# Kernel tuning notes

Measured on AMD Instinct MI355X. Metric: run time of the kernel, lower is better.

## Reference

```python
import jax, jax.numpy as jnp
import numpy as np

D_MODEL = 512
D_PROJ = 32
N_CENT = 6
CORR_HIDDEN = max(D_MODEL // 16, 32)  # 32
LN_EPS = 1e-5
ALPHA_DIR = 5.0


def _layernorm(x, g, b):
    mu = x.mean(axis=-1, keepdims=True)
    var = jnp.mean((x - mu) ** 2, axis=-1, keepdims=True)
    return (x - mu) * jax.lax.rsqrt(var + LN_EPS) * g + b


def _l2norm(x, eps=1e-12):
    n = jnp.sqrt(jnp.sum(x * x, axis=-1, keepdims=True))
    return x / jnp.maximum(n, eps)


def setup_inputs() -> dict:
    key = jax.random.key(0)
    ks = jax.random.split(key, 8)
    B, N = 64, 1024
    x = jax.random.normal(ks[0], (B, N, D_MODEL), dtype=jnp.float32)
    s_in = 1.0 / np.sqrt(D_MODEL)
    proj_w = jax.random.uniform(ks[1], (D_PROJ, D_MODEL), jnp.float32, -s_in, s_in)
    proj_b = jax.random.uniform(ks[2], (D_PROJ,), jnp.float32, -s_in, s_in)
    ln_g = jnp.ones((D_PROJ,), jnp.float32)
    ln_b = jnp.zeros((D_PROJ,), jnp.float32)
    centroids = jax.random.uniform(ks[3], (N_CENT, D_PROJ), jnp.float32, -3.0, 3.0)
    s_c = 1.0 / np.sqrt(D_MODEL + D_PROJ)
    corr_in_w = jax.random.uniform(ks[4], (CORR_HIDDEN, D_MODEL + D_PROJ), jnp.float32, -s_c, s_c)
    corr_in_b = jax.random.uniform(ks[5], (CORR_HIDDEN,), jnp.float32, -s_c, s_c)
    # correction_out is zero-init in the module; use small random values so the
    # correction path is numerically exercised by the baseline.
    corr_out_w = jax.random.normal(ks[6], (D_MODEL, CORR_HIDDEN), jnp.float32) * 0.02
    corr_out_b = jax.random.normal(ks[7], (D_MODEL,), jnp.float32) * 0.02
    return {
        "x": x, "proj_w": proj_w, "proj_b": proj_b, "ln_g": ln_g, "ln_b": ln_b,
        "centroids": centroids,
        "corr_in_w": corr_in_w, "corr_in_b": corr_in_b,
        "corr_out_w": corr_out_w, "corr_out_b": corr_out_b,
        "gate_alpha": jnp.float32(0.0),
        "routing_log_temp": jnp.float32(1.6),
        "scale_evidence": jnp.float32(5.0),
    }


def reference(x, proj_w, proj_b, ln_g, ln_b, centroids, corr_in_w, corr_in_b,
              corr_out_w, corr_out_b, gate_alpha, routing_log_temp, scale_evidence):
    B, N, D = x.shape
    # per-variate RevIN-style normalization over the variate axis (dim=1), unbiased std
    rev_mean = x.mean(axis=1, keepdims=True)
    rev_var = jnp.sum((x - rev_mean) ** 2, axis=1, keepdims=True) / (N - 1)
    rev_std = jnp.sqrt(rev_var) + 1e-5
    x_norm = (x - rev_mean) / rev_std
    # geometric routing: proj -> LN -> cosine sim against centroids
    Q = _layernorm(jnp.einsum("bnd,pd->bnp", x_norm, proj_w) + proj_b, ln_g, ln_b)
    Q_n = _l2norm(Q)                      # [B,N,P]
    K_n = _l2norm(centroids)              # [K,P]
    sim_cos = jnp.einsum("bnp,kp->bnk", Q_n, K_n)
    soft_assign = jax.nn.softmax(sim_cos * jnp.exp(routing_log_temp), axis=-1)
    centroid_ctx = jnp.einsum("bnk,kp->bnp", soft_assign, centroids)
    # centroid-conditioned correction MLP (dropout is identity in eval)
    corr_input = jnp.concatenate([x_norm, centroid_ctx], axis=-1)  # [B,N,D+P]
    h = jax.nn.gelu(jnp.einsum("bnc,hc->bnh", corr_input, corr_in_w) + corr_in_b, approximate=False)
    correction = (jnp.einsum("bnh,dh->bnd", h, corr_out_w) + corr_out_b) * rev_std
    gate = jax.nn.sigmoid(gate_alpha)
    out = x + gate * correction
    # DST uncertainty (no-grad diagnostic)
    sim_ctrl = jax.lax.stop_gradient(sim_cos)
    dir_gate = jax.nn.softplus((sim_ctrl - sim_ctrl.mean(axis=-1, keepdims=True)) * ALPHA_DIR)
    s_ev = jax.nn.softplus(jax.lax.stop_gradient(scale_evidence))
    S_train = jnp.sum(dir_gate * s_ev + 1.0, axis=-1, keepdims=True)
    u_std = N_CENT / S_train
    # losses
    gram = K_n @ K_n.T
    ortho_loss = jnp.mean((gram - jnp.eye(N_CENT, dtype=x.dtype)) ** 2)
    avg_routing = soft_assign.mean(axis=(0, 1))
    latent_loss = jnp.mean((avg_routing - 1.0 / N_CENT) ** 2)
    return out, u_std, ortho_loss, latent_loss
```

## Files before the change

kernel.cpp:

```cpp
#include <hip/hip_runtime.h>
#include <cstdint>
#include <cstddef>

#define N_DIM 1024
#define D_DIM 512
#define M_DIM 65536
#define NC 6

typedef float f32x4 __attribute__((ext_vector_type(4)));
typedef __bf16 bf16x8 __attribute__((ext_vector_type(8)));

__device__ __forceinline__ float sp_f(float z) {
    return z > 20.f ? z : log1pf(expf(z));
}

__global__ void k_pack(const float* __restrict__ pw, const float* __restrict__ ciw,
                       const float* __restrict__ cow, const float* __restrict__ cent,
                       const float* __restrict__ ga, const float* __restrict__ rlt,
                       const float* __restrict__ sev,
                       __bf16* __restrict__ bpa, __bf16* __restrict__ bpl,
                       __bf16* __restrict__ w3p,
                       float* __restrict__ kn, float* __restrict__ cw,
                       float* __restrict__ scal, float* __restrict__ out_ortho) {
    __shared__ float skn[NC * 32];
    __shared__ float ssq[36];
    int bid = blockIdx.x, tid = threadIdx.x;
    if (bid < 128) {
        int i = bid * 256 + tid;
        int c = i >> 9, k = i & 511;
        float w = (c < 32) ? pw[c * 512 + k] : ciw[(c - 32) * 544 + k];
        __bf16 hi = (__bf16)w;
        bpa[i] = hi;
        if (c < 32) bpl[i] = (__bf16)(w - (float)hi);
    } else if (bid < 192) {
        int j = (bid - 128) * 256 + tid;
        w3p[j] = (__bf16)cow[j];
    } else if (bid == 192) {
        if (tid < 192) {
            int k = tid >> 5, h = tid & 31;
            float s = 0.f;
            for (int p = 0; p < 32; ++p) s += cent[k * 32 + p] * ciw[h * 544 + 512 + p];
            cw[k * 32 + h] = s;
        } else if (tid < 192 + NC) {
            int k = tid - 192;
            float s = 0.f;
            for (int p = 0; p < 32; ++p) { float v = cent[k * 32 + p]; s += v * v; }
            float inv = 1.f / fmaxf(sqrtf(s), 1e-12f);
            for (int p = 0; p < 32; ++p) kn[k * 32 + p] = cent[k * 32 + p] * inv;
        } else if (tid == 198) {
            scal[0] = expf(rlt[0]);
            scal[1] = sp_f(sev[0]);
            scal[2] = 1.f / (1.f + expf(-ga[0]));
        }
    } else {
        if (tid < NC) {
            float s = 0.f;
            for (int p = 0; p < 32; ++p) { float v = cent[tid * 32 + p]; s += v * v; }
            float inv = 1.f / fmaxf(sqrtf(s), 1e-12f);
            for (int p = 0; p < 32; ++p) skn[tid * 32 + p] = cent[tid * 32 + p] * inv;
        }
        __syncthreads();
        if (tid < 36) {
            int i = tid / 6, j = tid % 6;
            float g = 0.f;
            for (int p = 0; p < 32; ++p) g += skn[i * 32 + p] * skn[j * 32 + p];
            float d = g - (i == j ? 1.f : 0.f);
            ssq[tid] = d * d;
        }
        __syncthreads();
        if (tid == 0) {
            float s = 0.f;
            for (int i = 0; i < 36; ++i) s += ssq[i];
            *out_ortho = s / 36.f;
        }
    }
}

__global__ void k_stat1(const float* __restrict__ x, float* __restrict__ part) {
    int bid = blockIdx.x;
    int b = bid >> 5, sub = bid & 31;
    int d4 = threadIdx.x * 4;
    const float* px = x + ((size_t)(b * 1024 + sub * 32)) * 512 + d4;
    f32x4 s = {0.f, 0.f, 0.f, 0.f}, q = s;
    #pragma unroll 8
    for (int i = 0; i < 32; ++i) {
        float4 v = *(const float4*)(px + (size_t)i * 512);
        s.x += v.x; s.y += v.y; s.z += v.z; s.w += v.w;
        q.x += v.x * v.x; q.y += v.y * v.y; q.z += v.z * v.z; q.w += v.w * v.w;
    }
    *(f32x4*)(part + (size_t)bid * 512 + d4) = s;
    *(f32x4*)(part + (size_t)(2048 + bid) * 512 + d4) = q;
}

__global__ void k_stat2(const float* __restrict__ part, float* __restrict__ mean,
                        float* __restrict__ istd, float* __restrict__ stdv) {
    int b = blockIdx.x, d = threadIdx.x;
    float s = 0.f, q = 0.f;
    for (int c = 0; c < 32; ++c) {
        s += part[(size_t)(b * 32 + c) * 512 + d];
        q += part[(size_t)(2048 + b * 32 + c) * 512 + d];
    }
    float mu = s * (1.f / (float)N_DIM);
    float var = fmaxf((q - s * mu) * (1.f / (float)(N_DIM - 1)), 0.f);
    float sd = sqrtf(var) + 1e-5f;
    mean[b * D_DIM + d] = mu;
    istd[b * D_DIM + d] = 1.f / sd;
    stdv[b * D_DIM + d] = sd;
}

__launch_bounds__(256)
__global__ void mega(const float* __restrict__ x,
                     const float* __restrict__ proj_b, const float* __restrict__ ln_g,
                     const float* __restrict__ ln_b, const float* __restrict__ cib,
                     const float* __restrict__ cob,
                     const float* __restrict__ mean, const float* __restrict__ istd,
                     const float* __restrict__ stdv,
                     const float* __restrict__ kn, const float* __restrict__ cw,
                     const float* __restrict__ scal,
                     const __bf16* __restrict__ bpa, const __bf16* __restrict__ bpl,
                     const __bf16* __restrict__ w3p,
                     float* __restrict__ out, float* __restrict__ ustd_out,
                     float* __restrict__ rout_part) {
    __shared__ float s_mean[512];
    __shared__ float s_is[512];
    __shared__ float s_sd[512];
    __shared__ float s_cob[512];
    __shared__ __align__(16) float s_tile[2][16][68];
    __shared__ __align__(16) __bf16 s_h[2][16][40];

    int tid = threadIdx.x;
    int wv = tid >> 6, ln = tid & 63;
    int l15 = ln & 15, lg = ln >> 4;
    int pair = wv >> 1, h = wv & 1;

    int b = blockIdx.x >> 5;
    int wrow = blockIdx.x * 32 + pair * 16;

    if (tid < 128) {
        *(float4*)&s_mean[tid * 4] = *(const float4*)(mean + b * 512 + tid * 4);
        *(float4*)&s_sd[tid * 4]   = *(const float4*)(stdv + b * 512 + tid * 4);
    } else {
        int t = tid - 128;
        *(float4*)&s_is[t * 4]  = *(const float4*)(istd + b * 512 + t * 4);
        *(float4*)&s_cob[t * 4] = *(const float4*)(cob + t * 4);
    }
    __syncthreads();

    int kbase = h * 256;
    const float* xr = x + (size_t)(wrow + l15) * 512 + kbase;
    const __bf16* w0  = bpa + (size_t)l15 * 512 + kbase;
    const __bf16* w1  = bpa + (size_t)(16 + l15) * 512 + kbase;
    const __bf16* w2  = bpa + (size_t)(32 + l15) * 512 + kbase;
    const __bf16* w3  = bpa + (size_t)(48 + l15) * 512 + kbase;
    const __bf16* wl0 = bpl + (size_t)l15 * 512 + kbase;
    const __bf16* wl1 = bpl + (size_t)(16 + l15) * 512 + kbase;

    f32x4 a0 = {0.f, 0.f, 0.f, 0.f}, a1 = a0, a2 = a0, a3 = a0;
    #pragma unroll
    for (int ks = 0; ks < 8; ++ks) {
        int k0 = ks * 32 + lg * 8;
        int kk = kbase + k0;
        float4 xa = *(const float4*)(xr + k0);
        float4 xb = *(const float4*)(xr + k0 + 4);
        float4 ma = *(const float4*)&s_mean[kk];
        float4 m2 = *(const float4*)&s_mean[kk + 4];
        float4 ia = *(const float4*)&s_is[kk];
        float4 i2 = *(const float4*)&s_is[kk + 4];
        float xnf[8];
        xnf[0] = (xa.x - ma.x) * ia.x; xnf[1] = (xa.y - ma.y) * ia.y;
        xnf[2] = (xa.z - ma.z) * ia.z; xnf[3] = (xa.w - ma.w) * ia.w;
        xnf[4] = (xb.x - m2.x) * i2.x; xnf[5] = (xb.y - m2.y) * i2.y;
        xnf[6] = (xb.z - m2.z) * i2.z; xnf[7] = (xb.w - m2.w) * i2.w;
        bf16x8 ah, al;
        #pragma unroll
        for (int j = 0; j < 8; ++j) {
            __bf16 hh = (__bf16)xnf[j];
            ah[j] = hh;
            al[j] = (__bf16)(xnf[j] - (float)hh);
        }
        bf16x8 wh0 = *(const bf16x8*)(w0 + k0);
        bf16x8 wh1 = *(const bf16x8*)(w1 + k0);
        a0 = __builtin_amdgcn_mfma_f32_16x16x32_bf16(ah, wh0, a0, 0, 0, 0);
        a0 = __builtin_amdgcn_mfma_f32_16x16x32_bf16(ah, *(const bf16x8*)(wl0 + k0), a0, 0, 0, 0);
        a0 = __builtin_amdgcn_mfma_f32_16x16x32_bf16(al, wh0, a0, 0, 0, 0);
        a1 = __builtin_amdgcn_mfma_f32_16x16x32_bf16(ah, wh1, a1, 0, 0, 0);
        a1 = __builtin_amdgcn_mfma_f32_16x16x32_bf16(ah, *(const bf16x8*)(wl1 + k0), a1, 0, 0, 0);
        a1 = __builtin_amdgcn_mfma_f32_16x16x32_bf16(al, wh1, a1, 0, 0, 0);
        a2 = __builtin_amdgcn_mfma_f32_16x16x32_bf16(ah, *(const bf16x8*)(w2 + k0), a2, 0, 0, 0);
        a3 = __builtin_amdgcn_mfma_f32_16x16x32_bf16(ah, *(const bf16x8*)(w3 + k0), a3, 0, 0, 0);
    }

    if (h == 1) {
        #pragma unroll
        for (int rg = 0; rg < 4; ++rg) {
            int row = lg * 4 + rg;
            s_tile[pair][row][l15]      = a0[rg];
            s_tile[pair][row][16 + l15] = a1[rg];
            s_tile[pair][row][32 + l15] = a2[rg];
            s_tile[pair][row][48 + l15] = a3[rg];
        }
    }
    __syncthreads();

    if (h == 0) {
        #pragma unroll
        for (int rg = 0; rg < 4; ++rg) {
            int row = lg * 4 + rg;
            s_tile[pair][row][l15]      += a0[rg];
            s_tile[pair][row][16 + l15] += a1[rg];
            s_tile[pair][row][32 + l15] += a2[rg];
            s_tile[pair][row][48 + l15] += a3[rg];
        }

        int r = ln >> 2, sub = ln & 3;
        const float* tr = &s_tile[pair][r][0];
        float4 t0 = *(const float4*)(tr + sub * 8);
        float4 t1 = *(const float4*)(tr + sub * 8 + 4);
        float4 pb0 = *(const float4*)(proj_b + sub * 8);
        float4 pb1 = *(const float4*)(proj_b + sub * 8 + 4);
        float P[8];
        P[0] = t0.x + pb0.x; P[1] = t0.y + pb0.y; P[2] = t0.z + pb0.z; P[3] = t0.w + pb0.w;
        P[4] = t1.x + pb1.x; P[5] = t1.y + pb1.y; P[6] = t1.z + pb1.z; P[7] = t1.w + pb1.w;
        float m = 0.f;
        #pragma unroll
        for (int j = 0; j < 8; ++j) m += P[j];
        m += __shfl_xor(m, 1); m += __shfl_xor(m, 2);
        float mu = m * (1.f / 32.f);
        float v = 0.f;
        #pragma unroll
        for (int j = 0; j < 8; ++j) { float d = P[j] - mu; v += d * d; }
        v += __shfl_xor(v, 1); v += __shfl_xor(v, 2);
        float rs = rsqrtf(v * (1.f / 32.f) + 1e-5f);
        float4 g0 = *(const float4*)(ln_g + sub * 8);
        float4 g1 = *(const float4*)(ln_g + sub * 8 + 4);
        float4 bl0 = *(const float4*)(ln_b + sub * 8);
        float4 bl1 = *(const float4*)(ln_b + sub * 8 + 4);
        float gg[8] = {g0.x, g0.y, g0.z, g0.w, g1.x, g1.y, g1.z, g1.w};
        float bb[8] = {bl0.x, bl0.y, bl0.z, bl0.w, bl1.x, bl1.y, bl1.z, bl1.w};
        float q[8]; float n2 = 0.f;
        #pragma unroll
        for (int j = 0; j < 8; ++j) {
            q[j] = (P[j] - mu) * rs * gg[j] + bb[j];
            n2 += q[j] * q[j];
        }
        n2 += __shfl_xor(n2, 1); n2 += __shfl_xor(n2, 2);
        float inv = 1.f / fmaxf(sqrtf(n2), 1e-12f);
        float sim[6];
        #pragma unroll
        for (int k = 0; k < 6; ++k) {
            const float* kr = kn + k * 32 + sub * 8;
            float4 ka = *(const float4*)(kr);
            float4 kb = *(const float4*)(kr + 4);
            float s = q[0] * ka.x + q[1] * ka.y + q[2] * ka.z + q[3] * ka.w
                    + q[4] * kb.x + q[5] * kb.y + q[6] * kb.z + q[7] * kb.w;
            s += __shfl_xor(s, 1); s += __shfl_xor(s, 2);
            sim[k] = s * inv;
        }
        float T = scal[0], sevv = scal[1];
        float mx = sim[0];
        #pragma unroll
        for (int k = 1; k < 6; ++k) mx = fmaxf(mx, sim[k]);
        float e[6], es = 0.f;
        #pragma unroll
        for (int k = 0; k < 6; ++k) { e[k] = expf((sim[k] - mx) * T); es += e[k]; }
        float einv = 1.f / es;
        float a[6];
        #pragma unroll
        for (int k = 0; k < 6; ++k) a[k] = e[k] * einv;
        float msim = 0.f;
        #pragma unroll
        for (int k = 0; k < 6; ++k) msim += sim[k];
        msim *= (1.f / 6.f);
        float S = 6.f;
        #pragma unroll
        for (int k = 0; k < 6; ++k) S += sevv * sp_f((sim[k] - msim) * 5.f);
        if (sub == 0) ustd_out[wrow + r] = 6.f / S;
        float4 h0 = *(const float4*)(tr + 32 + sub * 8);
        float4 h1 = *(const float4*)(tr + 32 + sub * 8 + 4);
        float4 c0 = *(const float4*)(cib + sub * 8);
        float4 c1 = *(const float4*)(cib + sub * 8 + 4);
        float vh[8] = {h0.x + c0.x, h0.y + c0.y, h0.z + c0.z, h0.w + c0.w,
                       h1.x + c1.x, h1.y + c1.y, h1.z + c1.z, h1.w + c1.w};
        #pragma unroll
        for (int k = 0; k < 6; ++k) {
            const float* cr = cw + k * 32 + sub * 8;
            float4 ca = *(const float4*)(cr);
            float4 cb = *(const float4*)(cr + 4);
            vh[0] += a[k] * ca.x; vh[1] += a[k] * ca.y; vh[2] += a[k] * ca.z; vh[3] += a[k] * ca.w;
            vh[4] += a[k] * cb.x; vh[5] += a[k] * cb.y; vh[6] += a[k] * cb.z; vh[7] += a[k] * cb.w;
        }
        bf16x8 hv;
        #pragma unroll
        for (int j = 0; j < 8; ++j) {
            float gv = 0.5f * vh[j] * (1.f + erff(vh[j] * 0.70710678118654752f));
            hv[j] = (__bf16)gv;
        }
        *(bf16x8*)(&s_h[pair][r][sub * 8]) = hv;
        #pragma unroll
        for (int k = 0; k < 6; ++k) {
            float rv = (sub == 0) ? a[k] : 0.f;
            rv += __shfl_xor(rv, 4); rv += __shfl_xor(rv, 8);
            rv += __shfl_xor(rv, 16); rv += __shfl_xor(rv, 32);
            if (ln == 0) atomicAdd(rout_part + (blockIdx.x & 63) * 6 + k, rv);
        }
    }
    __syncthreads();

    bf16x8 ha = *(const bf16x8*)(&s_h[pair][l15][lg * 8]);
    float gate = scal[2];
    int nf0 = h * 16;
    int row = wrow + l15;
    for (int nf = nf0; nf < nf0 + 16; ++nf) {
        int col = nf * 16 + l15;
        bf16x8 wb = *(const bf16x8*)(w3p + col * 32 + lg * 8);
        f32x4 z = {0.f, 0.f, 0.f, 0.f};
        f32x4 d = __builtin_amdgcn_mfma_f32_16x16x32_bf16(wb, ha, z, 0, 0, 0);
        int colb = nf * 16 + lg * 4;
        float4 xv = *(const float4*)(x + (size_t)row * 512 + colb);
        float4 bi = *(const float4*)&s_cob[colb];
        float4 sd = *(const float4*)&s_sd[colb];
        float4 o;
        o.x = xv.x + gate * ((d[0] + bi.x) * sd.x);
        o.y = xv.y + gate * ((d[1] + bi.y) * sd.y);
        o.z = xv.z + gate * ((d[2] + bi.z) * sd.z);
        o.w = xv.w + gate * ((d[3] + bi.w) * sd.w);
        *(float4*)(out + (size_t)row * 512 + colb) = o;
    }
}

__global__ void k5(const float* __restrict__ rp, float* __restrict__ out_latent) {
    __shared__ float sv[6];
    int t = threadIdx.x;
    if (t < 6) {
        float s = 0.f;
        for (int i = 0; i < 64; ++i) s += rp[i * 6 + t];
        sv[t] = s;
    }
    __syncthreads();
    if (t == 0) {
        float s = 0.f;
        for (int k = 0; k < 6; ++k) {
            float av = sv[k] * (1.f / (float)M_DIM) - (1.f / 6.f);
            s += av * av;
        }
        *out_latent = s / 6.f;
    }
}

extern "C" void kernel_launch(void* const* d_in, const int* in_sizes, int n_in,
                              void* d_out, int out_size, void* d_ws, size_t ws_size,
                              hipStream_t stream) {
    const float* x      = (const float*)d_in[0];
    const float* proj_w = (const float*)d_in[1];
    const float* proj_b = (const float*)d_in[2];
    const float* ln_g   = (const float*)d_in[3];
    const float* ln_b   = (const float*)d_in[4];
    const float* cent   = (const float*)d_in[5];
    const float* ciw    = (const float*)d_in[6];
    const float* cib    = (const float*)d_in[7];
    const float* cow    = (const float*)d_in[8];
    const float* cob    = (const float*)d_in[9];
    const float* ga     = (const float*)d_in[10];
    const float* rlt    = (const float*)d_in[11];
    const float* sev    = (const float*)d_in[12];

    char* ws = (char*)d_ws;
    float*  rout = (float*)(ws + 0);
    float*  kn   = (float*)(ws + 2048);
    float*  cwv  = (float*)(ws + 4096);
    float*  scal = (float*)(ws + 6144);
    __bf16* bpa  = (__bf16*)(ws + 8192);
    __bf16* bpl  = (__bf16*)(ws + 73728);
    __bf16* w3p  = (__bf16*)(ws + 106496);
    float*  mean = (float*)(ws + 139264);
    float*  istd = (float*)(ws + 270336);
    float*  stdv = (float*)(ws + 401408);

    float* outp   = (float*)d_out;
    float* ustd   = outp + (size_t)M_DIM * D_DIM;
    float* ortho  = ustd + M_DIM;
    float* latent = ortho + 1;

    float* part = (float*)d_out;

    hipMemsetAsync(rout, 0, 64 * 6 * sizeof(float), stream);
    k_pack<<<194, 256, 0, stream>>>(proj_w, ciw, cow, cent, ga, rlt, sev,
                                    bpa, bpl, w3p, kn, cwv, scal, ortho);
    k_stat1<<<2048, 128, 0, stream>>>(x, part);
    k_stat2<<<64, 512, 0, stream>>>(part, mean, istd, stdv);
    mega<<<2048, 256, 0, stream>>>(x, proj_b, ln_g, ln_b, cib, cob,
                                   mean, istd, stdv, kn, cwv, scal,
                                   bpa, bpl, w3p, outp, ustd, rout);
    k5<<<1, 64, 0, stream>>>(rout, latent);
}
```

Baseline: 140.3 us.

## Split K across four waves per 16-row tile and double grid size

Each block now handles 16 rows rather than 32. All four waves split the 512-wide K dimension of the projection GEMM, 128 columns each, and the partial results are reduced in shared memory by wave 0. The output stage spreads the 32 column fragments across the four waves and fully unrolls the loop. The grid doubles to 4096 blocks to raise parallelism and shorten per-wave serial work, at the cost of more per-block overhead: staging the per-batch stats again, extra syncs, and wave 0 doing the LayerNorm/routing tail alone while the other waves idle.

```diff
diff --git a/kernel.cpp b/kernel.cpp
--- a/kernel.cpp
+++ b/kernel.cpp
@@ -125,16 +125,15 @@
     __shared__ float s_is[512];
     __shared__ float s_sd[512];
     __shared__ float s_cob[512];
-    __shared__ __align__(16) float s_tile[2][16][68];
-    __shared__ __align__(16) __bf16 s_h[2][16][40];
+    __shared__ __align__(16) float s_t[3][16][68];
+    __shared__ __align__(16) __bf16 s_h[16][40];
 
     int tid = threadIdx.x;
     int wv = tid >> 6, ln = tid & 63;
     int l15 = ln & 15, lg = ln >> 4;
-    int pair = wv >> 1, h = wv & 1;
-
-    int b = blockIdx.x >> 5;
-    int wrow = blockIdx.x * 32 + pair * 16;
+
+    int b = blockIdx.x >> 6;
+    int wrow = blockIdx.x * 16;
 
     if (tid < 128) {
         *(float4*)&s_mean[tid * 4] = *(const float4*)(mean + b * 512 + tid * 4);
@@ -146,7 +145,7 @@
     }
     __syncthreads();
 
-    int kbase = h * 256;
+    int kbase = wv * 128;
     const float* xr = x + (size_t)(wrow + l15) * 512 + kbase;
     const __bf16* w0  = bpa + (size_t)l15 * 512 + kbase;
     const __bf16* w1  = bpa + (size_t)(16 + l15) * 512 + kbase;
@@ -157,7 +156,7 @@
 
     f32x4 a0 = {0.f, 0.f, 0.f, 0.f}, a1 = a0, a2 = a0, a3 = a0;
     #pragma unroll
-    for (int ks = 0; ks < 8; ++ks) {
+    for (int ks = 0; ks < 4; ++ks) {
         int k0 = ks * 32 + lg * 8;
         int kk = kbase + k0;
         float4 xa = *(const float4*)(xr + k0);
@@ -190,30 +189,35 @@
         a3 = __builtin_amdgcn_mfma_f32_16x16x32_bf16(ah, *(const bf16x8*)(w3 + k0), a3, 0, 0, 0);
     }
 
-    if (h == 1) {
+    if (wv != 0) {
+        int j = wv - 1;
         #pragma unroll
         for (int rg = 0; rg < 4; ++rg) {
             int row = lg * 4 + rg;
-            s_tile[pair][row][l15]      = a0[rg];
-            s_tile[pair][row][16 + l15] = a1[rg];
-            s_tile[pair][row][32 + l15] = a2[rg];
-            s_tile[pair][row][48 + l15] = a3[rg];
+            s_t[j][row][l15]      = a0[rg];
+            s_t[j][row][16 + l15] = a1[rg];
+            s_t[j][row][32 + l15] = a2[rg];
+            s_t[j][row][48 + l15] = a3[rg];
         }
     }
     __syncthreads();
 
-    if (h == 0) {
+    if (wv == 0) {
         #pragma unroll
         for (int rg = 0; rg < 4; ++rg) {
             int row = lg * 4 + rg;
-            s_tile[pair][row][l15]      += a0[rg];
-            s_tile[pair][row][16 + l15] += a1[rg];
-            s_tile[pair][row][32 + l15] += a2[rg];
-            s_tile[pair][row][48 + l15] += a3[rg];
+            a0[rg] += s_t[0][row][l15]      + s_t[1][row][l15]      + s_t[2][row][l15];
+            a1[rg] += s_t[0][row][16 + l15] + s_t[1][row][16 + l15] + s_t[2][row][16 + l15];
+            a2[rg] += s_t[0][row][32 + l15] + s_t[1][row][32 + l15] + s_t[2][row][32 + l15];
+            a3[rg] += s_t[0][row][48 + l15] + s_t[1][row][48 + l15] + s_t[2][row][48 + l15];
+            s_t[0][row][l15]      = a0[rg];
+            s_t[0][row][16 + l15] = a1[rg];
+            s_t[0][row][32 + l15] = a2[rg];
+            s_t[0][row][48 + l15] = a3[rg];
         }
 
         int r = ln >> 2, sub = ln & 3;
-        const float* tr = &s_tile[pair][r][0];
+        const float* tr = &s_t[0][r][0];
         float4 t0 = *(const float4*)(tr + sub * 8);
         float4 t1 = *(const float4*)(tr + sub * 8 + 4);
         float4 pb0 = *(const float4*)(proj_b + sub * 8);
@@ -295,7 +299,7 @@
             float gv = 0.5f * vh[j] * (1.f + erff(vh[j] * 0.70710678118654752f));
             hv[j] = (__bf16)gv;
         }
-        *(bf16x8*)(&s_h[pair][r][sub * 8]) = hv;
+        *(bf16x8*)(&s_h[r][sub * 8]) = hv;
         #pragma unroll
         for (int k = 0; k < 6; ++k) {
             float rv = (sub == 0) ? a[k] : 0.f;
@@ -306,25 +310,28 @@
     }
     __syncthreads();
 
-    bf16x8 ha = *(const bf16x8*)(&s_h[pair][l15][lg * 8]);
+    bf16x8 ha = *(const bf16x8*)(&s_h[l15][lg * 8]);
     float gate = scal[2];
-    int nf0 = h * 16;
     int row = wrow + l15;
-    for (int nf = nf0; nf < nf0 + 16; ++nf) {
+    const float* xrow = x + (size_t)row * 512;
+    float* orow = out + (size_t)row * 512;
+    #pragma unroll
+    for (int i = 0; i < 8; ++i) {
+        int nf = wv * 8 + i;
         int col = nf * 16 + l15;
         bf16x8 wb = *(const bf16x8*)(w3p + col * 32 + lg * 8);
         f32x4 z = {0.f, 0.f, 0.f, 0.f};
         f32x4 d = __builtin_amdgcn_mfma_f32_16x16x32_bf16(wb, ha, z, 0, 0, 0);
         int colb = nf * 16 + lg * 4;
-        float4 xv = *(const float4*)(x + (size_t)row * 512 + colb);
+        float4 xv = *(const float4*)(xrow + colb);
         float4 bi = *(const float4*)&s_cob[colb];
         float4 sd = *(const float4*)&s_sd[colb];
-        float4 o;
-        o.x = xv.x + gate * ((d[0] + bi.x) * sd.x);
-        o.y = xv.y + gate * ((d[1] + bi.y) * sd.y);
-        o.z = xv.z + gate * ((d[2] + bi.z) * sd.z);
-        o.w = xv.w + gate * ((d[3] + bi.w) * sd.w);
-        *(float4*)(out + (size_t)row * 512 + colb) = o;
+        f32x4 o;
+        o[0] = xv.x + gate * ((d[0] + bi.x) * sd.x);
+        o[1] = xv.y + gate * ((d[1] + bi.y) * sd.y);
+        o[2] = xv.z + gate * ((d[2] + bi.z) * sd.z);
+        o[3] = xv.w + gate * ((d[3] + bi.w) * sd.w);
+        *(f32x4*)(orow + colb) = o;
     }
 }
 
@@ -388,7 +395,7 @@
                                     bpa, bpl, w3p, kn, cwv, scal, ortho);
     k_stat1<<<2048, 128, 0, stream>>>(x, part);
     k_stat2<<<64, 512, 0, stream>>>(part, mean, istd, stdv);
-    mega<<<2048, 256, 0, stream>>>(x, proj_b, ln_g, ln_b, cib, cob,
+    mega<<<4096, 256, 0, stream>>>(x, proj_b, ln_g, ln_b, cib, cob,
                                    mean, istd, stdv, kn, cwv, scal,
                                    bpa, bpl, w3p, outp, ustd, rout);
     k5<<<1, 64, 0, stream>>>(rout, latent);
```

After: 146.4 us. +4.4%, slower.

## Fold RevIN normalization into per-batch weights and bias, precompute gated epilogue scales

Applied to the files above, without the earlier changes.

Adds a k_pack2 kernel that scales the projection and correction-input weights by each batch's inverse std and folds the mean term into per-batch bias vectors. The mega kernel can then feed raw x into the MFMAs without the per-element subtract and multiply, and its epilogue uses precomputed sd*gate and cob*sd*gate. Small constants (kn, cw, ln params, scalars) are staged in shared memory. The cost is an extra launch and a per-batch copy of the weights (about 4 MB of bf16) that mega must read, which means fewer cache hits across batches, plus a change in rounding because x is split into hi/lo before normalization.

```diff
diff --git a/kernel.cpp b/kernel.cpp
--- a/kernel.cpp
+++ b/kernel.cpp
@@ -18,24 +18,16 @@
                        const float* __restrict__ cow, const float* __restrict__ cent,
                        const float* __restrict__ ga, const float* __restrict__ rlt,
                        const float* __restrict__ sev,
-                       __bf16* __restrict__ bpa, __bf16* __restrict__ bpl,
-                       __bf16* __restrict__ w3p,
-                       float* __restrict__ kn, float* __restrict__ cw,
-                       float* __restrict__ scal, float* __restrict__ out_ortho) {
+                       __bf16* __restrict__ w3p, float* __restrict__ kn,
+                       float* __restrict__ cw, float* __restrict__ scal,
+                       float* __restrict__ out_ortho) {
     __shared__ float skn[NC * 32];
     __shared__ float ssq[36];
     int bid = blockIdx.x, tid = threadIdx.x;
-    if (bid < 128) {
-        int i = bid * 256 + tid;
-        int c = i >> 9, k = i & 511;
-        float w = (c < 32) ? pw[c * 512 + k] : ciw[(c - 32) * 544 + k];
-        __bf16 hi = (__bf16)w;
-        bpa[i] = hi;
-        if (c < 32) bpl[i] = (__bf16)(w - (float)hi);
-    } else if (bid < 192) {
-        int j = (bid - 128) * 256 + tid;
+    if (bid < 64) {
+        int j = bid * 256 + tid;
         w3p[j] = (__bf16)cow[j];
-    } else if (bid == 192) {
+    } else if (bid == 64) {
         if (tid < 192) {
             int k = tid >> 5, h = tid & 31;
             float s = 0.f;
@@ -108,23 +100,73 @@
     stdv[b * D_DIM + d] = sd;
 }
 
+__global__ void k_pack2(const float* __restrict__ pw, const float* __restrict__ ciw,
+                        const float* __restrict__ proj_b, const float* __restrict__ cib,
+                        const float* __restrict__ cob,
+                        const float* __restrict__ mean, const float* __restrict__ istd,
+                        const float* __restrict__ stdv, const float* __restrict__ scal,
+                        __bf16* __restrict__ bpa2, __bf16* __restrict__ bpl2,
+                        float* __restrict__ c2g, float* __restrict__ sdg,
+                        float* __restrict__ bsg) {
+    __shared__ float s_mi[512];
+    __shared__ float s_part[4][64];
+    int bid = blockIdx.x, tid = threadIdx.x;
+    int b = bid / 7, part = bid % 7;
+    if (part < 6) {
+        #pragma unroll
+        for (int r = 0; r < 16; ++r) {
+            int cc = part * 16 + r;
+            for (int k = tid; k < 512; k += 256) {
+                float is = istd[b * 512 + k];
+                if (cc < 64) {
+                    float w = (cc < 32) ? pw[cc * 512 + k] : ciw[(cc - 32) * 544 + k];
+                    bpa2[((size_t)b * 64 + cc) * 512 + k] = (__bf16)(w * is);
+                } else {
+                    int c0 = cc - 64;
+                    float v = pw[c0 * 512 + k] * is;
+                    __bf16 hi = (__bf16)v;
+                    bpl2[((size_t)b * 32 + c0) * 512 + k] = (__bf16)(v - (float)hi);
+                }
+            }
+        }
+    } else {
+        float g = scal[2];
+        for (int k = tid; k < 512; k += 256) {
+            s_mi[k] = mean[b * 512 + k] * istd[b * 512 + k];
+            float sd = stdv[b * 512 + k];
+            sdg[b * 512 + k] = sd * g;
+            bsg[b * 512 + k] = cob[k] * sd * g;
+        }
+        __syncthreads();
+        int col = tid & 63, seg = tid >> 6;
+        float s = 0.f;
+        for (int k = seg * 128; k < seg * 128 + 128; ++k) {
+            float w = (col < 32) ? pw[col * 512 + k] : ciw[(col - 32) * 544 + k];
+            s += s_mi[k] * w;
+        }
+        s_part[seg][col] = s;
+        __syncthreads();
+        if (tid < 64) {
+            float bias = (tid < 32) ? proj_b[tid] : cib[tid - 32];
+            c2g[b * 64 + tid] = bias - (s_part[0][tid] + s_part[1][tid] +
+                                        s_part[2][tid] + s_part[3][tid]);
+        }
+    }
+}
+
 __launch_bounds__(256)
 __global__ void mega(const float* __restrict__ x,
-                     const float* __restrict__ proj_b, const float* __restrict__ ln_g,
-                     const float* __restrict__ ln_b, const float* __restrict__ cib,
-                     const float* __restrict__ cob,
-                     const float* __restrict__ mean, const float* __restrict__ istd,
-                     const float* __restrict__ stdv,
+                     const float* __restrict__ ln_g, const float* __restrict__ ln_b,
                      const float* __restrict__ kn, const float* __restrict__ cw,
-                     const float* __restrict__ scal,
-                     const __bf16* __restrict__ bpa, const __bf16* __restrict__ bpl,
+                     const float* __restrict__ scal, const float* __restrict__ c2g,
+                     const float* __restrict__ sdg, const float* __restrict__ bsg,
+                     const __bf16* __restrict__ bpa2, const __bf16* __restrict__ bpl2,
                      const __bf16* __restrict__ w3p,
                      float* __restrict__ out, float* __restrict__ ustd_out,
                      float* __restrict__ rout_part) {
-    __shared__ float s_mean[512];
-    __shared__ float s_is[512];
-    __shared__ float s_sd[512];
-    __shared__ float s_cob[512];
+    __shared__ float s_sdg[512];
+    __shared__ float s_bsg[512];
+    __shared__ float s_kn[192], s_cw[192], s_c2[64], s_g[32], s_bl[32], s_scal[3];
     __shared__ __align__(16) float s_tile[2][16][68];
     __shared__ __align__(16) __bf16 s_h[2][16][40];
 
@@ -137,46 +179,42 @@
     int wrow = blockIdx.x * 32 + pair * 16;
 
     if (tid < 128) {
-        *(float4*)&s_mean[tid * 4] = *(const float4*)(mean + b * 512 + tid * 4);
-        *(float4*)&s_sd[tid * 4]   = *(const float4*)(stdv + b * 512 + tid * 4);
+        *(float4*)&s_sdg[tid * 4] = *(const float4*)(sdg + b * 512 + tid * 4);
+        if (tid < 48)       *(float4*)&s_kn[tid * 4] = *(const float4*)(kn + tid * 4);
+        else if (tid < 96)  *(float4*)&s_cw[(tid - 48) * 4] = *(const float4*)(cw + (tid - 48) * 4);
+        else if (tid < 112) *(float4*)&s_c2[(tid - 96) * 4] = *(const float4*)(c2g + b * 64 + (tid - 96) * 4);
+        else if (tid < 120) *(float4*)&s_g[(tid - 112) * 4] = *(const float4*)(ln_g + (tid - 112) * 4);
+        else                *(float4*)&s_bl[(tid - 120) * 4] = *(const float4*)(ln_b + (tid - 120) * 4);
     } else {
-        int t = tid - 128;
-        *(float4*)&s_is[t * 4]  = *(const float4*)(istd + b * 512 + t * 4);
-        *(float4*)&s_cob[t * 4] = *(const float4*)(cob + t * 4);
+        *(float4*)&s_bsg[(tid - 128) * 4] = *(const float4*)(bsg + b * 512 + (tid - 128) * 4);
+        if (tid == 128) { s_scal[0] = scal[0]; s_scal[1] = scal[1]; s_scal[2] = scal[2]; }
     }
     __syncthreads();
 
     int kbase = h * 256;
     const float* xr = x + (size_t)(wrow + l15) * 512 + kbase;
-    const __bf16* w0  = bpa + (size_t)l15 * 512 + kbase;
-    const __bf16* w1  = bpa + (size_t)(16 + l15) * 512 + kbase;
-    const __bf16* w2  = bpa + (size_t)(32 + l15) * 512 + kbase;
-    const __bf16* w3  = bpa + (size_t)(48 + l15) * 512 + kbase;
-    const __bf16* wl0 = bpl + (size_t)l15 * 512 + kbase;
-    const __bf16* wl1 = bpl + (size_t)(16 + l15) * 512 + kbase;
+    const __bf16* wbase = bpa2 + ((size_t)b * 64) * 512 + kbase;
+    const __bf16* w0 = wbase + (size_t)l15 * 512;
+    const __bf16* w1 = wbase + (size_t)(16 + l15) * 512;
+    const __bf16* w2 = wbase + (size_t)(32 + l15) * 512;
+    const __bf16* w3 = wbase + (size_t)(48 + l15) * 512;
+    const __bf16* lbase = bpl2 + ((size_t)b * 32) * 512 + kbase;
+    const __bf16* wl0 = lbase + (size_t)l15 * 512;
+    const __bf16* wl1 = lbase + (size_t)(16 + l15) * 512;
 
     f32x4 a0 = {0.f, 0.f, 0.f, 0.f}, a1 = a0, a2 = a0, a3 = a0;
     #pragma unroll
     for (int ks = 0; ks < 8; ++ks) {
         int k0 = ks * 32 + lg * 8;
-        int kk = kbase + k0;
         float4 xa = *(const float4*)(xr + k0);
         float4 xb = *(const float4*)(xr + k0 + 4);
-        float4 ma = *(const float4*)&s_mean[kk];
-        float4 m2 = *(const float4*)&s_mean[kk + 4];
-        float4 ia = *(const float4*)&s_is[kk];
-        float4 i2 = *(const float4*)&s_is[kk + 4];
-        float xnf[8];
-        xnf[0] = (xa.x - ma.x) * ia.x; xnf[1] = (xa.y - ma.y) * ia.y;
-        xnf[2] = (xa.z - ma.z) * ia.z; xnf[3] = (xa.w - ma.w) * ia.w;
-        xnf[4] = (xb.x - m2.x) * i2.x; xnf[5] = (xb.y - m2.y) * i2.y;
-        xnf[6] = (xb.z - m2.z) * i2.z; xnf[7] = (xb.w - m2.w) * i2.w;
+        float xf[8] = {xa.x, xa.y, xa.z, xa.w, xb.x, xb.y, xb.z, xb.w};
         bf16x8 ah, al;
         #pragma unroll
         for (int j = 0; j < 8; ++j) {
-            __bf16 hh = (__bf16)xnf[j];
+            __bf16 hh = (__bf16)xf[j];
             ah[j] = hh;
-            al[j] = (__bf16)(xnf[j] - (float)hh);
+            al[j] = (__bf16)(xf[j] - (float)hh);
         }
         bf16x8 wh0 = *(const bf16x8*)(w0 + k0);
         bf16x8 wh1 = *(const bf16x8*)(w1 + k0);
@@ -216,11 +254,11 @@
         const float* tr = &s_tile[pair][r][0];
         float4 t0 = *(const float4*)(tr + sub * 8);
         float4 t1 = *(const float4*)(tr + sub * 8 + 4);
-        float4 pb0 = *(const float4*)(proj_b + sub * 8);
-        float4 pb1 = *(const float4*)(proj_b + sub * 8 + 4);
+        float4 c2a = *(const float4*)&s_c2[sub * 8];
+        float4 c2b = *(const float4*)&s_c2[sub * 8 + 4];
         float P[8];
-        P[0] = t0.x + pb0.x; P[1] = t0.y + pb0.y; P[2] = t0.z + pb0.z; P[3] = t0.w + pb0.w;
-        P[4] = t1.x + pb1.x; P[5] = t1.y + pb1.y; P[6] = t1.z + pb1.z; P[7] = t1.w + pb1.w;
+        P[0] = t0.x + c2a.x; P[1] = t0.y + c2a.y; P[2] = t0.z + c2a.z; P[3] = t0.w + c2a.w;
+        P[4] = t1.x + c2b.x; P[5] = t1.y + c2b.y; P[6] = t1.z + c2b.z; P[7] = t1.w + c2b.w;
         float m = 0.f;
         #pragma unroll
         for (int j = 0; j < 8; ++j) m += P[j];
@@ -231,10 +269,10 @@
         for (int j = 0; j < 8; ++j) { float d = P[j] - mu; v += d * d; }
         v += __shfl_xor(v, 1); v += __shfl_xor(v, 2);
         float rs = rsqrtf(v * (1.f / 32.f) + 1e-5f);
-        float4 g0 = *(const float4*)(ln_g + sub * 8);
-        float4 g1 = *(const float4*)(ln_g + sub * 8 + 4);
-        float4 bl0 = *(const float4*)(ln_b + sub * 8);
-        float4 bl1 = *(const float4*)(ln_b + sub * 8 + 4);
+        float4 g0 = *(const float4*)&s_g[sub * 8];
+        float4 g1 = *(const float4*)&s_g[sub * 8 + 4];
+        float4 bl0 = *(const float4*)&s_bl[sub * 8];
+        float4 bl1 = *(const float4*)&s_bl[sub * 8 + 4];
         float gg[8] = {g0.x, g0.y, g0.z, g0.w, g1.x, g1.y, g1.z, g1.w};
         float bb[8] = {bl0.x, bl0.y, bl0.z, bl0.w, bl1.x, bl1.y, bl1.z, bl1.w};
         float q[8]; float n2 = 0.f;
@@ -248,7 +286,7 @@
         float sim[6];
         #pragma unroll
         for (int k = 0; k < 6; ++k) {
-            const float* kr = kn + k * 32 + sub * 8;
+            const float* kr = &s_kn[k * 32 + sub * 8];
             float4 ka = *(const float4*)(kr);
             float4 kb = *(const float4*)(kr + 4);
             float s = q[0] * ka.x + q[1] * ka.y + q[2] * ka.z + q[3] * ka.w
@@ -256,7 +294,7 @@
             s += __shfl_xor(s, 1); s += __shfl_xor(s, 2);
             sim[k] = s * inv;
         }
-        float T = scal[0], sevv = scal[1];
+        float T = s_scal[0], sevv = s_scal[1];
         float mx = sim[0];
         #pragma unroll
         for (int k = 1; k < 6; ++k) mx = fmaxf(mx, sim[k]);
@@ -277,13 +315,13 @@
         if (sub == 0) ustd_out[wrow + r] = 6.f / S;
         float4 h0 = *(const float4*)(tr + 32 + sub * 8);
         float4 h1 = *(const float4*)(tr + 32 + sub * 8 + 4);
-        float4 c0 = *(const float4*)(cib + sub * 8);
-        float4 c1 = *(const float4*)(cib + sub * 8 + 4);
+        float4 c0 = *(const float4*)&s_c2[32 + sub * 8];
+        float4 c1 = *(const float4*)&s_c2[32 + sub * 8 + 4];
         float vh[8] = {h0.x + c0.x, h0.y + c0.y, h0.z + c0.z, h0.w + c0.w,
                        h1.x + c1.x, h1.y + c1.y, h1.z + c1.z, h1.w + c1.w};
         #pragma unroll
         for (int k = 0; k < 6; ++k) {
-            const float* cr = cw + k * 32 + sub * 8;
+            const float* cr = &s_cw[k * 32 + sub * 8];
             float4 ca = *(const float4*)(cr);
             float4 cb = *(const float4*)(cr + 4);
             vh[0] += a[k] * ca.x; vh[1] += a[k] * ca.y; vh[2] += a[k] * ca.z; vh[3] += a[k] * ca.w;
@@ -307,7 +345,6 @@
     __syncthreads();
 
     bf16x8 ha = *(const bf16x8*)(&s_h[pair][l15][lg * 8]);
-    float gate = scal[2];
     int nf0 = h * 16;
     int row = wrow + l15;
     for (int nf = nf0; nf < nf0 + 16; ++nf) {
@@ -317,14 +354,14 @@
         f32x4 d = __builtin_amdgcn_mfma_f32_16x16x32_bf16(wb, ha, z, 0, 0, 0);
         int colb = nf * 16 + lg * 4;
         float4 xv = *(const float4*)(x + (size_t)row * 512 + colb);
-        float4 bi = *(const float4*)&s_cob[colb];
-        float4 sd = *(const float4*)&s_sd[colb];
-        float4 o;
-        o.x = xv.x + gate * ((d[0] + bi.x) * sd.x);
-        o.y = xv.y + gate * ((d[1] + bi.y) * sd.y);
-        o.z = xv.z + gate * ((d[2] + bi.z) * sd.z);
-        o.w = xv.w + gate * ((d[3] + bi.w) * sd.w);
-        *(float4*)(out + (size_t)row * 512 + colb) = o;
+        float4 sg = *(const float4*)&s_sdg[colb];
+        float4 bg = *(const float4*)&s_bsg[colb];
+        f32x4 o;
+        o[0] = xv.x + d[0] * sg.x + bg.x;
+        o[1] = xv.y + d[1] * sg.y + bg.y;
+        o[2] = xv.z + d[2] * sg.z + bg.z;
+        o[3] = xv.w + d[3] * sg.w + bg.w;
+        *(f32x4*)(out + (size_t)row * 512 + colb) = o;
     }
 }
 
@@ -369,12 +406,15 @@
     float*  kn   = (float*)(ws + 2048);
     float*  cwv  = (float*)(ws + 4096);
     float*  scal = (float*)(ws + 6144);
-    __bf16* bpa  = (__bf16*)(ws + 8192);
-    __bf16* bpl  = (__bf16*)(ws + 73728);
-    __bf16* w3p  = (__bf16*)(ws + 106496);
-    float*  mean = (float*)(ws + 139264);
-    float*  istd = (float*)(ws + 270336);
-    float*  stdv = (float*)(ws + 401408);
+    __bf16* w3p  = (__bf16*)(ws + 8192);
+    float*  mean = (float*)(ws + 40960);
+    float*  istd = (float*)(ws + 172032);
+    float*  stdv = (float*)(ws + 303104);
+    float*  sdg  = (float*)(ws + 434176);
+    float*  bsg  = (float*)(ws + 565248);
+    float*  c2g  = (float*)(ws + 696320);
+    __bf16* bpa2 = (__bf16*)(ws + 712704);
+    __bf16* bpl2 = (__bf16*)(ws + 4907008);
 
     float* outp   = (float*)d_out;
     float* ustd   = outp + (size_t)M_DIM * D_DIM;
@@ -384,12 +424,14 @@
     float* part = (float*)d_out;
 
     hipMemsetAsync(rout, 0, 64 * 6 * sizeof(float), stream);
-    k_pack<<<194, 256, 0, stream>>>(proj_w, ciw, cow, cent, ga, rlt, sev,
-                                    bpa, bpl, w3p, kn, cwv, scal, ortho);
+    k_pack<<<66, 256, 0, stream>>>(proj_w, ciw, cow, cent, ga, rlt, sev,
+                                   w3p, kn, cwv, scal, ortho);
     k_stat1<<<2048, 128, 0, stream>>>(x, part);
     k_stat2<<<64, 512, 0, stream>>>(part, mean, istd, stdv);
-    mega<<<2048, 256, 0, stream>>>(x, proj_b, ln_g, ln_b, cib, cob,
-                                   mean, istd, stdv, kn, cwv, scal,
-                                   bpa, bpl, w3p, outp, ustd, rout);
+    k_pack2<<<448, 256, 0, stream>>>(proj_w, ciw, proj_b, cib, cob,
+                                     mean, istd, stdv, scal,
+                                     bpa2, bpl2, c2g, sdg, bsg);
+    mega<<<2048, 256, 0, stream>>>(x, ln_g, ln_b, kn, cwv, scal, c2g, sdg, bsg,
+                                   bpa2, bpl2, w3p, outp, ustd, rout);
     k5<<<1, 64, 0, stream>>>(rout, latent);
 }
```

After: 189.9 us. 35.4% more time.
